# Performance work log

Measured on AMD Instinct MI355X. Metric: run time of the kernel, lower is better.

## Reference

```python
import jax, jax.numpy as jnp
import numpy as np

NUM_HEADS = 16
EMBED_DIM = 2048
HEAD_DIM = EMBED_DIM // NUM_HEADS        # 128
LATENT_DIM = HEAD_DIM // 4               # 32
GROUPS = HEAD_DIM // LATENT_DIM          # 4 latent sub-heads per q head
B, T = 1, 2048


def setup_inputs() -> dict:
    key = jax.random.key(0)
    ks = jax.random.split(key, 7)
    s_in = 1.0 / np.sqrt(EMBED_DIM)
    x = jax.random.normal(ks[0], (B, T, EMBED_DIM), dtype=jnp.float32)
    # torch Linear weights: [out_features, in_features]
    Wq = jax.random.normal(ks[1], (EMBED_DIM, EMBED_DIM), dtype=jnp.float32) * s_in
    Wk = jax.random.normal(ks[2], (EMBED_DIM, EMBED_DIM), dtype=jnp.float32) * s_in
    Wv = jax.random.normal(ks[3], (EMBED_DIM, EMBED_DIM), dtype=jnp.float32) * s_in
    Wlk = jax.random.normal(ks[4], (NUM_HEADS * LATENT_DIM, EMBED_DIM), dtype=jnp.float32) * s_in
    Wlv = jax.random.normal(ks[5], (NUM_HEADS * LATENT_DIM, EMBED_DIM), dtype=jnp.float32) * s_in
    Wo = jax.random.normal(ks[6], (EMBED_DIM, EMBED_DIM), dtype=jnp.float32) * s_in
    return {"x": x, "Wq": Wq, "Wk": Wk, "Wv": Wv, "Wlk": Wlk, "Wlv": Wlv, "Wo": Wo}


def reference(x, Wq, Wk, Wv, Wlk, Wlv, Wo):
    Bv, Tv, C = x.shape
    # q: [B,T,H,G,Dl]  (each head's 128-dim q split into 4 latent sub-heads)
    q = (x @ Wq.T).reshape(Bv, Tv, NUM_HEADS, GROUPS, LATENT_DIM)
    # latent k/v: [B,T,H,Dl], shared across the G sub-heads of each q head
    lk = (x @ Wlk.T).reshape(Bv, Tv, NUM_HEADS, LATENT_DIM)
    lv = (x @ Wlv.T).reshape(Bv, Tv, NUM_HEADS, LATENT_DIM)
    # k_proj / v_proj outputs are computed but unused in the original forward.
    scale = 1.0 / np.sqrt(HEAD_DIM).astype(np.float32)
    # scores: [B,H,G,T,T]
    scores = jnp.einsum('bthgd,bshd->bhgts', q, lk) * scale
    probs = jax.nn.softmax(scores, axis=-1)
    out = jnp.einsum('bhgts,bshd->bthgd', probs, lv).reshape(Bv, Tv, C)
    return out @ Wo.T
```

## Files before the change

### kernel.cpp

```cpp
#include <hip/hip_runtime.h>
#include <hip/hip_bf16.h>

typedef __bf16 bf16;
typedef __bf16 bf16x4 __attribute__((ext_vector_type(4)));
typedef __bf16 bf16x8 __attribute__((ext_vector_type(8)));
typedef float  f32x4  __attribute__((ext_vector_type(4)));

#define AS1 __attribute__((address_space(1)))
#define AS3 __attribute__((address_space(3)))

__device__ __forceinline__ void gload_lds16(const bf16* g, bf16* l) {
    __builtin_amdgcn_global_load_lds((const AS1 void*)g, (AS3 void*)l, 16, 0, 0);
}

__device__ __forceinline__ void stage8_f32(const float* s, bf16* l) {
    float4 a = *(const float4*)s;
    float4 b = *(const float4*)(s + 4);
    bf16x8 o;
    o[0] = (bf16)a.x; o[1] = (bf16)a.y; o[2] = (bf16)a.z; o[3] = (bf16)a.w;
    o[4] = (bf16)b.x; o[5] = (bf16)b.y; o[6] = (bf16)b.z; o[7] = (bf16)b.w;
    *(bf16x8*)l = o;
}

template <bool AF32, bool BF32>
__device__ __forceinline__ void gemm_core(
    const void* __restrict__ Av, const void* __restrict__ Bv,
    int m0, int n0, int K, f32x4 (&acc)[4][4],
    int wm, int wn, int r16, int q8)
{
    constexpr int LDA = AF32 ? 40 : 32;
    constexpr int LDB = BF32 ? 40 : 32;
    __shared__ __align__(16) bf16 As[2][128 * LDA];
    __shared__ __align__(16) bf16 Bs[2][128 * LDB];

    const int tid = threadIdx.x;
    const int i0 = tid, i1 = tid + 256;
    const int r0 = i0 >> 2, c0 = (i0 & 3) * 8;
    const int r1 = i1 >> 2, c1 = (i1 & 3) * 8;
    const size_t a0 = (size_t)(m0 + r0) * K + c0, a1 = (size_t)(m0 + r1) * K + c1;
    const size_t b0 = (size_t)(n0 + r0) * K + c0, b1 = (size_t)(n0 + r1) * K + c1;

    auto stage = [&](int buf, int k0) {
        if constexpr (AF32) {
            stage8_f32((const float*)Av + a0 + k0, &As[buf][r0 * LDA + c0]);
            stage8_f32((const float*)Av + a1 + k0, &As[buf][r1 * LDA + c1]);
        } else {
            gload_lds16((const bf16*)Av + a0 + k0, &As[buf][i0 * 8]);
            gload_lds16((const bf16*)Av + a1 + k0, &As[buf][i1 * 8]);
        }
        if constexpr (BF32) {
            stage8_f32((const float*)Bv + b0 + k0, &Bs[buf][r0 * LDB + c0]);
            stage8_f32((const float*)Bv + b1 + k0, &Bs[buf][r1 * LDB + c1]);
        } else {
            gload_lds16((const bf16*)Bv + b0 + k0, &Bs[buf][i0 * 8]);
            gload_lds16((const bf16*)Bv + b1 + k0, &Bs[buf][i1 * 8]);
        }
    };

    stage(0, 0);
    __syncthreads();

    int cur = 0;
    for (int k0 = 0; k0 < K; k0 += 32) {
        if (k0 + 32 < K) stage(cur ^ 1, k0 + 32);

        bf16x8 a[4], b[4];
#pragma unroll
        for (int r = 0; r < 4; ++r)
            a[r] = *(const bf16x8*)&As[cur][(wm + r * 16 + r16) * LDA + q8 * 8];
#pragma unroll
        for (int c = 0; c < 4; ++c)
            b[c] = *(const bf16x8*)&Bs[cur][(wn + c * 16 + r16) * LDB + q8 * 8];
#pragma unroll
        for (int r = 0; r < 4; ++r)
#pragma unroll
            for (int c = 0; c < 4; ++c)
                acc[r][c] = __builtin_amdgcn_mfma_f32_16x16x32_bf16(a[r], b[c], acc[r][c], 0, 0, 0);

        asm volatile("s_waitcnt vmcnt(0) lgkmcnt(0)" ::: "memory");
        __builtin_amdgcn_s_barrier();
        __builtin_amdgcn_sched_barrier(0);
        cur ^= 1;
    }
}

__global__ __launch_bounds__(256) void cvt5(
    const float* __restrict__ s0, const float* __restrict__ s1,
    const float* __restrict__ s2, const float* __restrict__ s3,
    const float* __restrict__ s4,
    bf16* __restrict__ d0, bf16* __restrict__ d1, bf16* __restrict__ d2,
    bf16* __restrict__ d3, bf16* __restrict__ d4)
{
    const float* S[5] = {s0, s1, s2, s3, s4};
    bf16*        D[5] = {d0, d1, d2, d3, d4};
    const int    N[5] = {4194304, 4194304, 1048576, 1048576, 4194304};
    int y = blockIdx.y;
    int base = (blockIdx.x * 256 + threadIdx.x) * 8;
    if (base >= N[y]) return;
    stage8_f32(S[y] + base, D[y] + base);
}

template <bool F32>
__global__ __launch_bounds__(256) void proj_kernel_t(
    const void* __restrict__ x, const void* __restrict__ Wq,
    const void* __restrict__ Wlk, const void* __restrict__ Wlv,
    bf16* __restrict__ Q, bf16* __restrict__ LK, bf16* __restrict__ LVt)
{
    const int bx = blockIdx.x, by = blockIdx.y;
    const int tid = threadIdx.x, lane = tid & 63, wave = tid >> 6;
    const int wm = (wave >> 1) * 64, wn = (wave & 1) * 64;
    const int r16 = lane & 15, q8 = lane >> 4;
    f32x4 acc[4][4] = {};

    const void* Bv; int n0;
    if (bx < 16)      { Bv = Wq;  n0 = bx * 128; }
    else if (bx < 20) { Bv = Wlk; n0 = (bx - 16) * 128; }
    else              { Bv = Wlv; n0 = (bx - 20) * 128; }

    gemm_core<F32, F32>(x, Bv, by * 128, n0, 2048, acc, wm, wn, r16, q8);

    if (bx < 20) {
        bf16* C  = (bx < 16) ? Q : LK;
        int ldc  = (bx < 16) ? 2048 : 512;
        const float sc = (bx < 16) ? 0.08838834764831845f * 1.4426950408889634f : 1.0f;
#pragma unroll
        for (int r = 0; r < 4; ++r)
#pragma unroll
            for (int c = 0; c < 4; ++c)
#pragma unroll
                for (int i = 0; i < 4; ++i) {
                    int row = by * 128 + wm + r * 16 + q8 * 4 + i;
                    int col = n0 + wn + c * 16 + r16;
                    C[(size_t)row * ldc + col] = (bf16)(acc[r][c][i] * sc);
                }
    } else {
#pragma unroll
        for (int r = 0; r < 4; ++r)
#pragma unroll
            for (int c = 0; c < 4; ++c) {
                int hd = n0 + wn + c * 16 + r16;
                int tb = by * 128 + wm + r * 16 + q8 * 4;
                bf16x4 pk;
#pragma unroll
                for (int i = 0; i < 4; ++i) pk[i] = (bf16)acc[r][c][i];
                *(bf16x4*)&LVt[(size_t)hd * 2048 + tb] = pk;
            }
    }
}

template <bool BF32>
__global__ __launch_bounds__(256) void out_kernel_t(
    const bf16* __restrict__ A, const void* __restrict__ Wo, float* __restrict__ C)
{
    const int tid = threadIdx.x, lane = tid & 63, wave = tid >> 6;
    const int wm = (wave >> 1) * 64, wn = (wave & 1) * 64;
    const int r16 = lane & 15, q8 = lane >> 4;
    f32x4 acc[4][4] = {};
    gemm_core<false, BF32>(A, Wo, blockIdx.y * 128, blockIdx.x * 128, 2048, acc, wm, wn, r16, q8);
#pragma unroll
    for (int r = 0; r < 4; ++r)
#pragma unroll
        for (int c = 0; c < 4; ++c)
#pragma unroll
            for (int i = 0; i < 4; ++i) {
                int row = blockIdx.y * 128 + wm + r * 16 + q8 * 4 + i;
                int col = blockIdx.x * 128 + wn + c * 16 + r16;
                C[(size_t)row * 2048 + col] = acc[r][c][i];
            }
}

__global__ __launch_bounds__(256) void attn5(
    const bf16* __restrict__ Q, const bf16* __restrict__ LK,
    const bf16* __restrict__ LVt, bf16* __restrict__ O)
{
    __shared__ __align__(16) bf16 Ks[2][64 * 32];
    __shared__ __align__(16) bf16 Vs[2][32 * 64];
    __shared__ __align__(16) bf16 Ps[256 * 72];

    const int tid  = threadIdx.x;
    const int lane = tid & 63;
    const int w    = tid >> 6;
    const int r16  = lane & 15;
    const int q8   = lane >> 4;
    const int hg = blockIdx.y, h = hg >> 2, g = hg & 3;
    const int t0 = blockIdx.x * 256;

    bf16x8 qb[4];
#pragma unroll
    for (int p = 0; p < 4; ++p)
        qb[p] = *(const bf16x8*)(Q + (size_t)(t0 + w * 64 + p * 16 + r16) * 2048
                                 + h * 128 + g * 32 + q8 * 8);

    const int kr = tid >> 2;
    const int kq = (tid & 3) ^ ((tid >> 3) & 3);
    const bf16* kg = LK + (size_t)kr * 512 + h * 32 + kq * 8;
    const int vd = tid >> 3;
    const int vq = (tid & 7) ^ ((tid >> 3) & 7);
    const bf16* vg = LVt + (size_t)(h * 32 + vd) * 2048 + vq * 8;

    const int ksw = (r16 >> 1) & 3;
    const int vsw = r16 & 7;

    f32x4 o_acc[4][2] = {};
    float lsum[4] = {0.f, 0.f, 0.f, 0.f};
    const f32x4 z = {0.f, 0.f, 0.f, 0.f};

    gload_lds16(kg, &Ks[0][tid * 8]);
    gload_lds16(vg, &Vs[0][tid * 8]);
    __syncthreads();

    int cur = 0;
    for (int sb = 0; sb < 2048; sb += 64) {
        if (sb + 64 < 2048) {
            gload_lds16(kg + (size_t)(sb + 64) * 512, &Ks[cur ^ 1][tid * 8]);
            gload_lds16(vg + (sb + 64),               &Vs[cur ^ 1][tid * 8]);
        }
        const bf16* ks = Ks[cur];
        const bf16* vs = Vs[cur];

        bf16x8 kb[4], vb[2][2];
#pragma unroll
        for (int c = 0; c < 4; ++c)
            kb[c] = *(const bf16x8*)&ks[(c * 16 + r16) * 32 + (q8 ^ ksw) * 8];
#pragma unroll
        for (int kk = 0; kk < 2; ++kk)
#pragma unroll
            for (int ct = 0; ct < 2; ++ct)
                vb[kk][ct] = *(const bf16x8*)&vs[(ct * 16 + r16) * 64
                                                 + (((kk * 4 + q8) ^ vsw) * 8)];

#pragma unroll
        for (int p = 0; p < 4; ++p) {
            f32x4 s[4];
            __builtin_amdgcn_s_setprio(1);
#pragma unroll
            for (int c = 0; c < 4; ++c)
                s[c] = __builtin_amdgcn_mfma_f32_16x16x32_bf16(kb[c], qb[p], z, 0, 0, 0);
            __builtin_amdgcn_s_setprio(0);
#pragma unroll
            for (int c = 0; c < 4; ++c) {
                bf16x4 pk;
#pragma unroll
                for (int i = 0; i < 4; ++i) {
                    float pv = exp2f(s[c][i]);
                    lsum[p] += pv;
                    pk[i] = (bf16)pv;
                }
                *(bf16x4*)&Ps[(size_t)(p * 64 + w * 16 + r16) * 72 + c * 16 + q8 * 4] = pk;
            }
            __builtin_amdgcn_s_setprio(1);
#pragma unroll
            for (int kk = 0; kk < 2; ++kk) {
                bf16x8 ap = *(const bf16x8*)&Ps[(size_t)(p * 64 + w * 16 + r16) * 72
                                                + kk * 32 + q8 * 8];
#pragma unroll
                for (int ct = 0; ct < 2; ++ct)
                    o_acc[p][ct] = __builtin_amdgcn_mfma_f32_16x16x32_bf16(ap, vb[kk][ct], o_acc[p][ct], 0, 0, 0);
            }
            __builtin_amdgcn_s_setprio(0);
        }

        asm volatile("s_waitcnt vmcnt(0) lgkmcnt(0)" ::: "memory");
        __builtin_amdgcn_s_barrier();
        __builtin_amdgcn_sched_barrier(0);
        cur ^= 1;
    }

#pragma unroll
    for (int p = 0; p < 4; ++p) {
        float l = lsum[p];
        l += __shfl_xor(l, 16);
        l += __shfl_xor(l, 32);
        float ls[4];
#pragma unroll
        for (int i = 0; i < 4; ++i) ls[i] = __shfl(l, q8 * 4 + i);
#pragma unroll
        for (int ct = 0; ct < 2; ++ct)
#pragma unroll
            for (int i = 0; i < 4; ++i) {
                float o = o_acc[p][ct][i] / ls[i];
                int t = t0 + w * 64 + p * 16 + q8 * 4 + i;
                int d = ct * 16 + r16;
                O[(size_t)t * 2048 + h * 128 + g * 32 + d] = (bf16)o;
            }
    }
}

extern "C" void kernel_launch(void* const* d_in, const int* in_sizes, int n_in,
                              void* d_out, int out_size, void* d_ws, size_t ws_size,
                              hipStream_t stream) {
    const float* x   = (const float*)d_in[0];
    const float* Wq  = (const float*)d_in[1];
    const float* Wlk = (const float*)d_in[4];
    const float* Wlv = (const float*)d_in[5];
    const float* Wo  = (const float*)d_in[6];
    float* out = (float*)d_out;

    const size_t M4 = 4194304, M1 = 1048576;
    const size_t need_fast = (M1 + M1 + M4 + M4 + M1 + M1) * 2;

    if (ws_size >= need_fast) {
        bf16* xb   = (bf16*)d_out;
        bf16* Wqb  = xb + M4;
        bf16* p    = (bf16*)d_ws;
        bf16* Wlkb = p; p += M1;
        bf16* Wlvb = p; p += M1;
        bf16* Wob  = p; p += M4;
        bf16* Qp   = p; p += M4;
        bf16* LKp  = p; p += M1;
        bf16* LVt  = p;
        bf16* ATT  = Qp;

        cvt5<<<dim3(2048, 5), 256, 0, stream>>>(x, Wq, Wlk, Wlv, Wo,
                                                xb, Wqb, Wlkb, Wlvb, Wob);
        proj_kernel_t<false><<<dim3(24, 16), 256, 0, stream>>>(xb, Wqb, Wlkb, Wlvb,
                                                               Qp, LKp, LVt);
        attn5<<<dim3(8, 64), 256, 0, stream>>>(Qp, LKp, LVt, ATT);
        out_kernel_t<false><<<dim3(16, 16), 256, 0, stream>>>(ATT, Wob, out);
    } else {
        bf16* Qp  = (bf16*)d_ws;
        bf16* LKp = Qp + M4;
        bf16* LVt = LKp + M1;
        bf16* ATT = Qp;

        proj_kernel_t<true><<<dim3(24, 16), 256, 0, stream>>>(x, Wq, Wlk, Wlv,
                                                              Qp, LKp, LVt);
        attn5<<<dim3(8, 64), 256, 0, stream>>>(Qp, LKp, LVt, ATT);
        out_kernel_t<true><<<dim3(16, 16), 256, 0, stream>>>(ATT, Wo, out);
    }
}
```

Measured before the change: 312.2 us.

## Halve GEMM and attention tiles for more blocks; MFMA row sums, swizzled P

The projection and output GEMMs switch from 128x128 to 128x64 tiles, which doubles the grid so more workgroups fill the GPU's CUs. The attention kernel now handles 128 query rows per block instead of 256 and gets a launch bound of 4 blocks per CU. It also stores P with an XOR swizzle instead of padding and computes the softmax denominator with an extra MFMA against a ones vector, replacing the scalar sums and shuffles. The cost is lower per-block data reuse in the GEMMs and one extra MFMA per P tile.

```diff
diff --git a/kernel.cpp b/kernel.cpp
--- a/kernel.cpp
+++ b/kernel.cpp
@@ -23,37 +23,37 @@
 }
 
 template <bool AF32, bool BF32>
-__device__ __forceinline__ void gemm_core(
+__device__ __forceinline__ void gemm_core64(
     const void* __restrict__ Av, const void* __restrict__ Bv,
-    int m0, int n0, int K, f32x4 (&acc)[4][4],
-    int wm, int wn, int r16, int q8)
+    int m0, int n0, int K, f32x4 (&acc)[2][4],
+    int wm, int r16, int q8)
 {
     constexpr int LDA = AF32 ? 40 : 32;
     constexpr int LDB = BF32 ? 40 : 32;
     __shared__ __align__(16) bf16 As[2][128 * LDA];
-    __shared__ __align__(16) bf16 Bs[2][128 * LDB];
+    __shared__ __align__(16) bf16 Bs[2][64 * LDB];
 
     const int tid = threadIdx.x;
     const int i0 = tid, i1 = tid + 256;
-    const int r0 = i0 >> 2, c0 = (i0 & 3) * 8;
-    const int r1 = i1 >> 2, c1 = (i1 & 3) * 8;
-    const size_t a0 = (size_t)(m0 + r0) * K + c0, a1 = (size_t)(m0 + r1) * K + c1;
-    const size_t b0 = (size_t)(n0 + r0) * K + c0, b1 = (size_t)(n0 + r1) * K + c1;
+    const int rA0 = i0 >> 2, rA1 = i1 >> 2;
+    const int rB  = tid >> 2;
+    const int c0  = (tid & 3) * 8;
+    const size_t a0 = (size_t)(m0 + rA0) * K + c0;
+    const size_t a1 = (size_t)(m0 + rA1) * K + c0;
+    const size_t b0 = (size_t)(n0 + rB)  * K + c0;
 
     auto stage = [&](int buf, int k0) {
         if constexpr (AF32) {
-            stage8_f32((const float*)Av + a0 + k0, &As[buf][r0 * LDA + c0]);
-            stage8_f32((const float*)Av + a1 + k0, &As[buf][r1 * LDA + c1]);
+            stage8_f32((const float*)Av + a0 + k0, &As[buf][rA0 * LDA + c0]);
+            stage8_f32((const float*)Av + a1 + k0, &As[buf][rA1 * LDA + c0]);
         } else {
             gload_lds16((const bf16*)Av + a0 + k0, &As[buf][i0 * 8]);
             gload_lds16((const bf16*)Av + a1 + k0, &As[buf][i1 * 8]);
         }
         if constexpr (BF32) {
-            stage8_f32((const float*)Bv + b0 + k0, &Bs[buf][r0 * LDB + c0]);
-            stage8_f32((const float*)Bv + b1 + k0, &Bs[buf][r1 * LDB + c1]);
+            stage8_f32((const float*)Bv + b0 + k0, &Bs[buf][rB * LDB + c0]);
         } else {
-            gload_lds16((const bf16*)Bv + b0 + k0, &Bs[buf][i0 * 8]);
-            gload_lds16((const bf16*)Bv + b1 + k0, &Bs[buf][i1 * 8]);
+            gload_lds16((const bf16*)Bv + b0 + k0, &Bs[buf][tid * 8]);
         }
     };
 
@@ -64,15 +64,15 @@
     for (int k0 = 0; k0 < K; k0 += 32) {
         if (k0 + 32 < K) stage(cur ^ 1, k0 + 32);
 
-        bf16x8 a[4], b[4];
-#pragma unroll
-        for (int r = 0; r < 4; ++r)
+        bf16x8 a[2], b[4];
+#pragma unroll
+        for (int r = 0; r < 2; ++r)
             a[r] = *(const bf16x8*)&As[cur][(wm + r * 16 + r16) * LDA + q8 * 8];
 #pragma unroll
         for (int c = 0; c < 4; ++c)
-            b[c] = *(const bf16x8*)&Bs[cur][(wn + c * 16 + r16) * LDB + q8 * 8];
-#pragma unroll
-        for (int r = 0; r < 4; ++r)
+            b[c] = *(const bf16x8*)&Bs[cur][(c * 16 + r16) * LDB + q8 * 8];
+#pragma unroll
+        for (int r = 0; r < 2; ++r)
 #pragma unroll
             for (int c = 0; c < 4; ++c)
                 acc[r][c] = __builtin_amdgcn_mfma_f32_16x16x32_bf16(a[r], b[c], acc[r][c], 0, 0, 0);
@@ -108,37 +108,37 @@
 {
     const int bx = blockIdx.x, by = blockIdx.y;
     const int tid = threadIdx.x, lane = tid & 63, wave = tid >> 6;
-    const int wm = (wave >> 1) * 64, wn = (wave & 1) * 64;
+    const int wm = wave * 32;
     const int r16 = lane & 15, q8 = lane >> 4;
-    f32x4 acc[4][4] = {};
+    f32x4 acc[2][4] = {};
 
     const void* Bv; int n0;
-    if (bx < 16)      { Bv = Wq;  n0 = bx * 128; }
-    else if (bx < 20) { Bv = Wlk; n0 = (bx - 16) * 128; }
-    else              { Bv = Wlv; n0 = (bx - 20) * 128; }
-
-    gemm_core<F32, F32>(x, Bv, by * 128, n0, 2048, acc, wm, wn, r16, q8);
-
-    if (bx < 20) {
-        bf16* C  = (bx < 16) ? Q : LK;
-        int ldc  = (bx < 16) ? 2048 : 512;
-        const float sc = (bx < 16) ? 0.08838834764831845f * 1.4426950408889634f : 1.0f;
-#pragma unroll
-        for (int r = 0; r < 4; ++r)
+    if (bx < 32)      { Bv = Wq;  n0 = bx * 64; }
+    else if (bx < 40) { Bv = Wlk; n0 = (bx - 32) * 64; }
+    else              { Bv = Wlv; n0 = (bx - 40) * 64; }
+
+    gemm_core64<F32, F32>(x, Bv, by * 128, n0, 2048, acc, wm, r16, q8);
+
+    if (bx < 40) {
+        bf16* C  = (bx < 32) ? Q : LK;
+        int ldc  = (bx < 32) ? 2048 : 512;
+        const float sc = (bx < 32) ? 0.08838834764831845f * 1.4426950408889634f : 1.0f;
+#pragma unroll
+        for (int r = 0; r < 2; ++r)
 #pragma unroll
             for (int c = 0; c < 4; ++c)
 #pragma unroll
                 for (int i = 0; i < 4; ++i) {
                     int row = by * 128 + wm + r * 16 + q8 * 4 + i;
-                    int col = n0 + wn + c * 16 + r16;
+                    int col = n0 + c * 16 + r16;
                     C[(size_t)row * ldc + col] = (bf16)(acc[r][c][i] * sc);
                 }
     } else {
 #pragma unroll
-        for (int r = 0; r < 4; ++r)
+        for (int r = 0; r < 2; ++r)
 #pragma unroll
             for (int c = 0; c < 4; ++c) {
-                int hd = n0 + wn + c * 16 + r16;
+                int hd = n0 + c * 16 + r16;
                 int tb = by * 128 + wm + r * 16 + q8 * 4;
                 bf16x4 pk;
 #pragma unroll
@@ -153,29 +153,29 @@
     const bf16* __restrict__ A, const void* __restrict__ Wo, float* __restrict__ C)
 {
     const int tid = threadIdx.x, lane = tid & 63, wave = tid >> 6;
-    const int wm = (wave >> 1) * 64, wn = (wave & 1) * 64;
+    const int wm = wave * 32;
     const int r16 = lane & 15, q8 = lane >> 4;
-    f32x4 acc[4][4] = {};
-    gemm_core<false, BF32>(A, Wo, blockIdx.y * 128, blockIdx.x * 128, 2048, acc, wm, wn, r16, q8);
-#pragma unroll
-    for (int r = 0; r < 4; ++r)
+    f32x4 acc[2][4] = {};
+    gemm_core64<false, BF32>(A, Wo, blockIdx.y * 128, blockIdx.x * 64, 2048, acc, wm, r16, q8);
+#pragma unroll
+    for (int r = 0; r < 2; ++r)
 #pragma unroll
         for (int c = 0; c < 4; ++c)
 #pragma unroll
             for (int i = 0; i < 4; ++i) {
                 int row = blockIdx.y * 128 + wm + r * 16 + q8 * 4 + i;
-                int col = blockIdx.x * 128 + wn + c * 16 + r16;
+                int col = blockIdx.x * 64 + c * 16 + r16;
                 C[(size_t)row * 2048 + col] = acc[r][c][i];
             }
 }
 
-__global__ __launch_bounds__(256) void attn5(
+__global__ __launch_bounds__(256, 4) void attn6(
     const bf16* __restrict__ Q, const bf16* __restrict__ LK,
     const bf16* __restrict__ LVt, bf16* __restrict__ O)
 {
     __shared__ __align__(16) bf16 Ks[2][64 * 32];
     __shared__ __align__(16) bf16 Vs[2][32 * 64];
-    __shared__ __align__(16) bf16 Ps[256 * 72];
+    __shared__ __align__(16) bf16 Ps[128 * 64];
 
     const int tid  = threadIdx.x;
     const int lane = tid & 63;
@@ -183,12 +183,12 @@
     const int r16  = lane & 15;
     const int q8   = lane >> 4;
     const int hg = blockIdx.y, h = hg >> 2, g = hg & 3;
-    const int t0 = blockIdx.x * 256;
-
-    bf16x8 qb[4];
-#pragma unroll
-    for (int p = 0; p < 4; ++p)
-        qb[p] = *(const bf16x8*)(Q + (size_t)(t0 + w * 64 + p * 16 + r16) * 2048
+    const int t0 = blockIdx.x * 128;
+
+    bf16x8 qb[2];
+#pragma unroll
+    for (int p = 0; p < 2; ++p)
+        qb[p] = *(const bf16x8*)(Q + (size_t)(t0 + w * 32 + p * 16 + r16) * 2048
                                  + h * 128 + g * 32 + q8 * 8);
 
     const int kr = tid >> 2;
@@ -201,8 +201,18 @@
     const int ksw = (r16 >> 1) & 3;
     const int vsw = r16 & 7;
 
-    f32x4 o_acc[4][2] = {};
-    float lsum[4] = {0.f, 0.f, 0.f, 0.f};
+    const int pk7 = r16 & 7;
+    const int ph  = q8 >> 1;
+    const int plo = (q8 & 1) * 4;
+    const int pb0 = ((w * 2 + 0) * 16 + r16) * 64;
+    const int pb1 = ((w * 2 + 1) * 16 + r16) * 64;
+
+    bf16x8 ones;
+#pragma unroll
+    for (int j = 0; j < 8; ++j) ones[j] = (bf16)1.0f;
+
+    f32x4 o_acc[2][2] = {};
+    f32x4 l_acc[2] = {};
     const f32x4 z = {0.f, 0.f, 0.f, 0.f};
 
     gload_lds16(kg, &Ks[0][tid * 8]);
@@ -230,7 +240,8 @@
                                                  + (((kk * 4 + q8) ^ vsw) * 8)];
 
 #pragma unroll
-        for (int p = 0; p < 4; ++p) {
+        for (int p = 0; p < 2; ++p) {
+            const int pbase = p ? pb1 : pb0;
             f32x4 s[4];
             __builtin_amdgcn_s_setprio(1);
 #pragma unroll
@@ -239,26 +250,27 @@
             __builtin_amdgcn_s_setprio(0);
 #pragma unroll
             for (int c = 0; c < 4; ++c) {
-                bf16x4 pk;
-#pragma unroll
-                for (int i = 0; i < 4; ++i) {
-                    float pv = exp2f(s[c][i]);
-                    lsum[p] += pv;
-                    pk[i] = (bf16)pv;
-                }
-                *(bf16x4*)&Ps[(size_t)(p * 64 + w * 16 + r16) * 72 + c * 16 + q8 * 4] = pk;
-            }
-            __builtin_amdgcn_s_setprio(1);
+                bf16x4 pkv;
+#pragma unroll
+                for (int i = 0; i < 4; ++i) pkv[i] = (bf16)exp2f(s[c][i]);
+                *(bf16x4*)&Ps[pbase + ((c * 2 + ph) ^ pk7) * 8 + plo] = pkv;
+            }
+        }
+
+        __builtin_amdgcn_s_setprio(1);
+#pragma unroll
+        for (int p = 0; p < 2; ++p) {
+            const int pbase = p ? pb1 : pb0;
 #pragma unroll
             for (int kk = 0; kk < 2; ++kk) {
-                bf16x8 ap = *(const bf16x8*)&Ps[(size_t)(p * 64 + w * 16 + r16) * 72
-                                                + kk * 32 + q8 * 8];
+                bf16x8 ap = *(const bf16x8*)&Ps[pbase + ((kk * 4 + q8) ^ pk7) * 8];
 #pragma unroll
                 for (int ct = 0; ct < 2; ++ct)
                     o_acc[p][ct] = __builtin_amdgcn_mfma_f32_16x16x32_bf16(ap, vb[kk][ct], o_acc[p][ct], 0, 0, 0);
-            }
-            __builtin_amdgcn_s_setprio(0);
-        }
+                l_acc[p] = __builtin_amdgcn_mfma_f32_16x16x32_bf16(ap, ones, l_acc[p], 0, 0, 0);
+            }
+        }
+        __builtin_amdgcn_s_setprio(0);
 
         asm volatile("s_waitcnt vmcnt(0) lgkmcnt(0)" ::: "memory");
         __builtin_amdgcn_s_barrier();
@@ -267,23 +279,17 @@
     }
 
 #pragma unroll
-    for (int p = 0; p < 4; ++p) {
-        float l = lsum[p];
-        l += __shfl_xor(l, 16);
-        l += __shfl_xor(l, 32);
-        float ls[4];
-#pragma unroll
-        for (int i = 0; i < 4; ++i) ls[i] = __shfl(l, q8 * 4 + i);
-#pragma unroll
-        for (int ct = 0; ct < 2; ++ct)
-#pragma unroll
-            for (int i = 0; i < 4; ++i) {
-                float o = o_acc[p][ct][i] / ls[i];
-                int t = t0 + w * 64 + p * 16 + q8 * 4 + i;
+    for (int p = 0; p < 2; ++p)
+#pragma unroll
+        for (int i = 0; i < 4; ++i) {
+            float inv = 1.0f / l_acc[p][i];
+            int t = t0 + w * 32 + p * 16 + q8 * 4 + i;
+#pragma unroll
+            for (int ct = 0; ct < 2; ++ct) {
                 int d = ct * 16 + r16;
-                O[(size_t)t * 2048 + h * 128 + g * 32 + d] = (bf16)o;
-            }
-    }
+                O[(size_t)t * 2048 + h * 128 + g * 32 + d] = (bf16)(o_acc[p][ct][i] * inv);
+            }
+        }
 }
 
 extern "C" void kernel_launch(void* const* d_in, const int* in_sizes, int n_in,
@@ -313,19 +319,19 @@
 
         cvt5<<<dim3(2048, 5), 256, 0, stream>>>(x, Wq, Wlk, Wlv, Wo,
                                                 xb, Wqb, Wlkb, Wlvb, Wob);
-        proj_kernel_t<false><<<dim3(24, 16), 256, 0, stream>>>(xb, Wqb, Wlkb, Wlvb,
+        proj_kernel_t<false><<<dim3(48, 16), 256, 0, stream>>>(xb, Wqb, Wlkb, Wlvb,
                                                                Qp, LKp, LVt);
-        attn5<<<dim3(8, 64), 256, 0, stream>>>(Qp, LKp, LVt, ATT);
-        out_kernel_t<false><<<dim3(16, 16), 256, 0, stream>>>(ATT, Wob, out);
+        attn6<<<dim3(16, 64), 256, 0, stream>>>(Qp, LKp, LVt, ATT);
+        out_kernel_t<false><<<dim3(32, 16), 256, 0, stream>>>(ATT, Wob, out);
     } else {
         bf16* Qp  = (bf16*)d_ws;
         bf16* LKp = Qp + M4;
         bf16* LVt = LKp + M1;
         bf16* ATT = Qp;
 
-        proj_kernel_t<true><<<dim3(24, 16), 256, 0, stream>>>(x, Wq, Wlk, Wlv,
+        proj_kernel_t<true><<<dim3(48, 16), 256, 0, stream>>>(x, Wq, Wlk, Wlv,
                                                               Qp, LKp, LVt);
-        attn5<<<dim3(8, 64), 256, 0, stream>>>(Qp, LKp, LVt, ATT);
-        out_kernel_t<true><<<dim3(16, 16), 256, 0, stream>>>(ATT, Wo, out);
+        attn6<<<dim3(16, 64), 256, 0, stream>>>(Qp, LKp, LVt, ATT);
+        out_kernel_t<true><<<dim3(32, 16), 256, 0, stream>>>(ATT, Wo, out);
     }
 }
```

New measurement: 284.6 us. 8.8% less time.
